# Kernel optimization log

Measured on AMD Instinct MI355X. Metric: run time of the kernel, lower is better.

Reference implementation:

```python
import jax, jax.numpy as jnp
import numpy as np

MIN_CLUSTERS = 3.0
MAX_CLUSTERS = 50.0


def setup_inputs() -> dict:
    key = jax.random.key(0)
    ks = jax.random.split(key, 8)
    B, N, D, H = 8, 100000, 64, 64
    E = 3200000
    x = jax.random.normal(ks[0], (B, N, D), dtype=jnp.float32)
    edge_index = jax.random.randint(ks[1], (2, E), 0, N, dtype=jnp.int64)
    in_dim = 3 * D + 4  # 196
    s1 = 1.0 / np.sqrt(in_dim)
    s2 = 1.0 / np.sqrt(H)
    s3 = 1.0 / np.sqrt(H // 2)
    W1 = jax.random.uniform(ks[2], (in_dim, H), jnp.float32, -s1, s1)
    b1 = jax.random.uniform(ks[3], (H,), jnp.float32, -s1, s1)
    W2 = jax.random.uniform(ks[4], (H, H // 2), jnp.float32, -s2, s2)
    b2 = jax.random.uniform(ks[5], (H // 2,), jnp.float32, -s2, s2)
    W3 = jax.random.uniform(ks[6], (H // 2, 1), jnp.float32, -s3, s3)
    b3 = jax.random.uniform(ks[7], (1,), jnp.float32, -s3, s3)
    return {"x": x, "edge_index": edge_index, "W1": W1, "b1": b1,
            "W2": W2, "b2": b2, "W3": W3, "b3": b3}


def reference(x, edge_index, W1, b1, W2, b2, W3, b3):
    B, N, D = x.shape
    # node pooling over the node axis (unbiased std, matching torch.std)
    x_mean = x.mean(axis=1)                 # [B, D]
    x_max = x.max(axis=1)                   # [B, D]
    x_std = jnp.std(x, axis=1, ddof=1)      # [B, D]
    # degree histogram: vectorized scatter-add replacing the serial python loop
    degrees = jnp.zeros((N,), dtype=jnp.float32).at[edge_index[1]].add(1.0)
    avg_degree = degrees.mean()
    std_degree = jnp.std(degrees, ddof=1)
    num_edges = edge_index.shape[1] // 2
    max_edges = N * (N - 1) / 2.0
    density = jnp.float32(num_edges / max_edges if max_edges > 0 else 0.0)
    normalized_size = jnp.float32(np.log(N + 1.0) / 10.0)
    structural = jnp.stack([avg_degree, std_degree, density, normalized_size])  # [4]
    structural = jnp.broadcast_to(structural[None, :], (B, 4))
    gf = jnp.concatenate([x_mean, x_max, x_std, structural], axis=1)  # [B, 3D+4]
    h = jax.nn.relu(gf @ W1 + b1)
    h = jax.nn.relu(h @ W2 + b2)
    cluster_raw = jax.nn.sigmoid(h @ W3 + b3)[:, 0]  # [B]
    cont = MIN_CLUSTERS + cluster_raw * (MAX_CLUSTERS - MIN_CLUSTERS)
    # straight-through round
    rounded = cont + jax.lax.stop_gradient(jnp.round(cont) - cont)
    return jnp.stack([rounded.mean(), cluster_raw.mean()])  # [num_clusters, raw_mean]
```

## Files before the change

kernel.cpp:

```cpp
#include <hip/hip_runtime.h>
#include <cstdint>
#include <cmath>


#define NSEG   64
#define NRNG   4
#define RBITS  15
#define RR     (1 << RBITS)
#define BPB    256
#define RFBLK  32

__device__ unsigned char      g_part[NSEG * NRNG * RR];
__device__ float              g_sum[512];
__device__ float              g_sq[512];
__device__ unsigned           g_max[512];
__device__ unsigned long long g_degSums[2];
__device__ unsigned           g_done = 0;

__device__ __forceinline__ unsigned enc_f32(float f) {
    unsigned u = __float_as_uint(f);
    return (u & 0x80000000u) ? ~u : (u | 0x80000000u);
}
__device__ __forceinline__ float dec_f32(unsigned u) {
    return (u & 0x80000000u) ? __uint_as_float(u ^ 0x80000000u) : __uint_as_float(~u);
}

__global__ __launch_bounds__(256) void hist_kernel(
    const int* __restrict__ ei, int E, int N)
{
    const int bid = blockIdx.x, tid = threadIdx.x;
    const int s = bid >> 2;
    const int p = bid & 3;
    const unsigned lo = (unsigned)p << RBITS;

    if (bid == 0) {
        for (int i = tid; i < 512; i += 256) { g_sum[i] = 0.f; g_sq[i] = 0.f; g_max[i] = 0u; }
        if (tid < 2) g_degSums[tid] = 0ull;
    }

    __shared__ unsigned h[RR];
    for (int i = tid; i < RR; i += 256) h[i] = 0u;
    __syncthreads();

    const int* row1 = ei + E;
    const int per = (E + NSEG - 1) / NSEG;
    const int elo = s * per, ehi = min(E, elo + per);
    const int span4 = (ehi - elo) & ~3;

    for (int i = elo + tid * 4; i + 3 < elo + span4 + 3 && i + 3 < ehi + 3 && i + 3 < elo + span4 + 4 && i < elo + span4; i += 256 * 4) {
        int4 v = *reinterpret_cast<const int4*>(row1 + i);
        unsigned r0 = (unsigned)v.x - lo; if (r0 < RR) atomicAdd(&h[r0], 1u);
        unsigned r1 = (unsigned)v.y - lo; if (r1 < RR) atomicAdd(&h[r1], 1u);
        unsigned r2 = (unsigned)v.z - lo; if (r2 < RR) atomicAdd(&h[r2], 1u);
        unsigned r3 = (unsigned)v.w - lo; if (r3 < RR) atomicAdd(&h[r3], 1u);
    }
    for (int i = elo + span4 + tid; i < ehi; i += 256) {
        unsigned r0 = (unsigned)row1[i] - lo; if (r0 < RR) atomicAdd(&h[r0], 1u);
    }
    __syncthreads();

    unsigned* outw = reinterpret_cast<unsigned*>(&g_part[(size_t)bid * RR]);
    for (int w = tid; w < RR / 4; w += 256) {
        unsigned c = (h[w*4] & 255u) | ((h[w*4+1] & 255u) << 8)
                   | ((h[w*4+2] & 255u) << 16) | ((h[w*4+3] & 255u) << 24);
        outw[w] = c;
    }
}

__global__ __launch_bounds__(256) void xstats_kernel(
    const float* __restrict__ x, int N, int rowsPerBlock)
{
    const int b   = blockIdx.x / BPB;
    const int blk = blockIdx.x - b * BPB;
    const int tid = threadIdx.x;
    const int d4  = tid & 15;
    const int rg  = tid >> 4;

    const int rowStart = blk * rowsPerBlock;
    const int rowEnd   = min(N, rowStart + rowsPerBlock);

    float s0 = 0.f, s1 = 0.f, s2 = 0.f, s3 = 0.f;
    float q0 = 0.f, q1 = 0.f, q2 = 0.f, q3 = 0.f;
    float m0 = -INFINITY, m1 = -INFINITY, m2 = -INFINITY, m3 = -INFINITY;

    const float* xb = x + (size_t)b * (size_t)N * 64 + d4 * 4;
    for (int r = rowStart + rg; r < rowEnd; r += 16) {
        float4 v = *reinterpret_cast<const float4*>(xb + (size_t)r * 64);
        s0 += v.x; s1 += v.y; s2 += v.z; s3 += v.w;
        q0 = fmaf(v.x, v.x, q0); q1 = fmaf(v.y, v.y, q1);
        q2 = fmaf(v.z, v.z, q2); q3 = fmaf(v.w, v.w, q3);
        m0 = fmaxf(m0, v.x); m1 = fmaxf(m1, v.y);
        m2 = fmaxf(m2, v.z); m3 = fmaxf(m3, v.w);
    }

    __shared__ float ls[256 * 4];
    __shared__ float lq[256 * 4];
    __shared__ float lm[256 * 4];
    ls[tid*4+0]=s0; ls[tid*4+1]=s1; ls[tid*4+2]=s2; ls[tid*4+3]=s3;
    lq[tid*4+0]=q0; lq[tid*4+1]=q1; lq[tid*4+2]=q2; lq[tid*4+3]=q3;
    lm[tid*4+0]=m0; lm[tid*4+1]=m1; lm[tid*4+2]=m2; lm[tid*4+3]=m3;
    __syncthreads();

    for (int off = 8; off; off >>= 1) {
        if (rg < off) {
            int o  = (tid + off * 16) * 4;
            int me = tid * 4;
            #pragma unroll
            for (int j = 0; j < 4; ++j) {
                ls[me+j] += ls[o+j];
                lq[me+j] += lq[o+j];
                lm[me+j]  = fmaxf(lm[me+j], lm[o+j]);
            }
        }
        __syncthreads();
    }

    if (rg == 0) {
        #pragma unroll
        for (int j = 0; j < 4; ++j) {
            int cell = b * 64 + d4 * 4 + j;
            atomicAdd(&g_sum[cell], ls[tid*4+j]);
            atomicAdd(&g_sq[cell],  lq[tid*4+j]);
            atomicMax(&g_max[cell], enc_f32(lm[tid*4+j]));
        }
    }
}

__global__ __launch_bounds__(256) void reduce_final_kernel(
    int N, long long E,
    const float* __restrict__ W1, const float* __restrict__ b1,
    const float* __restrict__ W2, const float* __restrict__ b2,
    const float* __restrict__ W3, const float* __restrict__ b3,
    float* __restrict__ out)
{
    const int bid = blockIdx.x, tid = threadIdx.x;
    const int p     = bid >> 3;
    const int chunk = bid & 7;

    uint4 acc = make_uint4(0u, 0u, 0u, 0u);
    const size_t roff = (size_t)chunk * 4096 + (size_t)tid * 16;
    for (int s = 0; s < NSEG; ++s) {
        const uint4 v = *reinterpret_cast<const uint4*>(
            &g_part[((size_t)(s * NRNG + p)) * RR + roff]);
        acc.x += v.x; acc.y += v.y; acc.z += v.z; acc.w += v.w;
    }
    unsigned sd = 0, sq = 0;
    unsigned words[4] = {acc.x, acc.y, acc.z, acc.w};
    #pragma unroll
    for (int wi = 0; wi < 4; ++wi) {
        #pragma unroll
        for (int by = 0; by < 4; ++by) {
            unsigned d = (words[wi] >> (by * 8)) & 255u;
            sd += d;
            sq += d * d;
        }
    }
    #pragma unroll
    for (int off = 32; off; off >>= 1) {
        sd += __shfl_down(sd, off, 64);
        sq += __shfl_down(sq, off, 64);
    }
    __shared__ unsigned wsd[4], wsq[4];
    if ((tid & 63) == 0) { wsd[tid >> 6] = sd; wsq[tid >> 6] = sq; }
    __syncthreads();
    if (tid == 0) {
        unsigned long long S = 0, Q = 0;
        #pragma unroll
        for (int wv = 0; wv < 4; ++wv) { S += wsd[wv]; Q += wsq[wv]; }
        atomicAdd(&g_degSums[0], S);
        atomicAdd(&g_degSums[1], Q);
    }

    __shared__ int lastFlag;
    __syncthreads();
    if (tid == 0) {
        unsigned old = atomicAdd(&g_done, 1u);
        lastFlag = (old == (unsigned)gridDim.x - 1u);
    }
    __syncthreads();
    if (!lastFlag) return;

    __shared__ float gf[8][200];
    __shared__ float h1s[8][64];
    __shared__ float h2s[8][32];
    __shared__ float raw[8], rnd[8];
    __shared__ unsigned long long degS[2];

    if (tid < 2) degS[tid] = atomicAdd(&g_degSums[tid], 0ull);
    __syncthreads();

    for (int i = tid; i < 512; i += 256) {
        int bb = i >> 6, d = i & 63;
        float sum = g_sum[i], sqv = g_sq[i];
        float mean = sum / (float)N;
        float var  = fmaxf(0.f, sqv - sum * sum / (float)N) / (float)(N - 1);
        gf[bb][d]       = mean;
        gf[bb][64 + d]  = dec_f32(g_max[i]);
        gf[bb][128 + d] = sqrtf(var);
    }
    if (tid < 32) {
        int bb = tid >> 2, k = tid & 3;
        double dsum = (double)degS[0];
        double dsq  = (double)degS[1];
        double avg  = dsum / (double)N;
        double var  = (dsq - dsum * dsum / (double)N) / (double)(N - 1);
        long long num_edges = E / 2;
        double max_edges = (double)N * (double)(N - 1) / 2.0;
        float v;
        if      (k == 0) v = (float)avg;
        else if (k == 1) v = (float)sqrt(var);
        else if (k == 2) v = (float)((double)num_edges / max_edges);
        else             v = (float)(log((double)N + 1.0) / 10.0);
        gf[bb][192 + k] = v;
    }
    __syncthreads();

    if (tid < 64) {
        int d = tid;
        for (int bb = 0; bb < 8; ++bb) {
            float acc2 = b1[d];
            for (int k = 0; k < 196; ++k)
                acc2 = fmaf(gf[bb][k], W1[k * 64 + d], acc2);
            h1s[bb][d] = fmaxf(acc2, 0.f);
        }
    }
    __syncthreads();

    if (tid < 32) {
        int d = tid;
        for (int bb = 0; bb < 8; ++bb) {
            float acc2 = b2[d];
            for (int k = 0; k < 64; ++k)
                acc2 = fmaf(h1s[bb][k], W2[k * 32 + d], acc2);
            h2s[bb][d] = fmaxf(acc2, 0.f);
        }
    }
    __syncthreads();

    if (tid < 8) {
        float acc2 = b3[0];
        for (int k = 0; k < 32; ++k)
            acc2 = fmaf(h2s[tid][k], W3[k], acc2);
        float r = 1.f / (1.f + expf(-acc2));
        raw[tid] = r;
        float cont = 3.0f + r * 47.0f;
        rnd[tid] = rintf(cont);
    }
    __syncthreads();

    if (tid == 0) {
        float sr = 0.f, sw = 0.f;
        for (int bb = 0; bb < 8; ++bb) { sr += rnd[bb]; sw += raw[bb]; }
        out[0] = sr * 0.125f;
        out[1] = sw * 0.125f;
        atomicExch(&g_done, 0u);
    }
}

extern "C" void kernel_launch(void* const* d_in, const int* in_sizes, int n_in,
                              void* d_out, int out_size, void* d_ws, size_t ws_size,
                              hipStream_t stream)
{
    const float* x  = (const float*)d_in[0];
    const int*   ei = (const int*)d_in[1];
    const float* W1 = (const float*)d_in[2];
    const float* b1 = (const float*)d_in[3];
    const float* W2 = (const float*)d_in[4];
    const float* b2 = (const float*)d_in[5];
    const float* W3 = (const float*)d_in[6];
    const float* b3 = (const float*)d_in[7];
    float* out = (float*)d_out;

    int N = in_sizes[0] / (8 * 64);
    if (N > NRNG * RR) N = NRNG * RR;
    const int E = in_sizes[1] / 2;

    const int rpb = (N + BPB - 1) / BPB;

    hist_kernel        <<<NSEG * NRNG, 256, 0, stream>>>(ei, E, N);
    xstats_kernel      <<<8 * BPB,     256, 0, stream>>>(x, N, rpb);
    reduce_final_kernel<<<RFBLK,       256, 0, stream>>>(N, (long long)E,
                                                         W1, b1, W2, b2, W3, b3, out);
}
```

Baseline: 131.8 us.

## Fuse x-statistics and degree reduction into one kernel with last-block finalize

```diff
diff --git a/kernel.cpp b/kernel.cpp
--- a/kernel.cpp
+++ b/kernel.cpp
@@ -8,6 +8,7 @@
 #define RBITS  15
 #define RR     (1 << RBITS)
 #define BPB    256
+#define XB     (8 * BPB)
 #define RFBLK  32
 
 __device__ unsigned char      g_part[NSEG * NRNG * RR];
@@ -45,17 +46,23 @@
     const int* row1 = ei + E;
     const int per = (E + NSEG - 1) / NSEG;
     const int elo = s * per, ehi = min(E, elo + per);
-    const int span4 = (ehi - elo) & ~3;
-
-    for (int i = elo + tid * 4; i + 3 < elo + span4 + 3 && i + 3 < ehi + 3 && i + 3 < elo + span4 + 4 && i < elo + span4; i += 256 * 4) {
-        int4 v = *reinterpret_cast<const int4*>(row1 + i);
-        unsigned r0 = (unsigned)v.x - lo; if (r0 < RR) atomicAdd(&h[r0], 1u);
-        unsigned r1 = (unsigned)v.y - lo; if (r1 < RR) atomicAdd(&h[r1], 1u);
-        unsigned r2 = (unsigned)v.z - lo; if (r2 < RR) atomicAdd(&h[r2], 1u);
-        unsigned r3 = (unsigned)v.w - lo; if (r3 < RR) atomicAdd(&h[r3], 1u);
-    }
-    for (int i = elo + span4 + tid; i < ehi; i += 256) {
-        unsigned r0 = (unsigned)row1[i] - lo; if (r0 < RR) atomicAdd(&h[r0], 1u);
+
+    if ((elo & 3) == 0) {
+        const int span4 = elo + ((ehi - elo) & ~3);
+        for (int i = elo + tid * 4; i < span4; i += 256 * 4) {
+            int4 v = *reinterpret_cast<const int4*>(row1 + i);
+            unsigned r0 = (unsigned)v.x - lo; if (r0 < RR) atomicAdd(&h[r0], 1u);
+            unsigned r1 = (unsigned)v.y - lo; if (r1 < RR) atomicAdd(&h[r1], 1u);
+            unsigned r2 = (unsigned)v.z - lo; if (r2 < RR) atomicAdd(&h[r2], 1u);
+            unsigned r3 = (unsigned)v.w - lo; if (r3 < RR) atomicAdd(&h[r3], 1u);
+        }
+        for (int i = span4 + tid; i < ehi; i += 256) {
+            unsigned r0 = (unsigned)row1[i] - lo; if (r0 < RR) atomicAdd(&h[r0], 1u);
+        }
+    } else {
+        for (int i = elo + tid; i < ehi; i += 256) {
+            unsigned r0 = (unsigned)row1[i] - lo; if (r0 < RR) atomicAdd(&h[r0], 1u);
+        }
     }
     __syncthreads();
 
@@ -67,111 +74,125 @@
     }
 }
 
-__global__ __launch_bounds__(256) void xstats_kernel(
-    const float* __restrict__ x, int N, int rowsPerBlock)
-{
-    const int b   = blockIdx.x / BPB;
-    const int blk = blockIdx.x - b * BPB;
-    const int tid = threadIdx.x;
-    const int d4  = tid & 15;
-    const int rg  = tid >> 4;
-
-    const int rowStart = blk * rowsPerBlock;
-    const int rowEnd   = min(N, rowStart + rowsPerBlock);
-
-    float s0 = 0.f, s1 = 0.f, s2 = 0.f, s3 = 0.f;
-    float q0 = 0.f, q1 = 0.f, q2 = 0.f, q3 = 0.f;
-    float m0 = -INFINITY, m1 = -INFINITY, m2 = -INFINITY, m3 = -INFINITY;
-
-    const float* xb = x + (size_t)b * (size_t)N * 64 + d4 * 4;
-    for (int r = rowStart + rg; r < rowEnd; r += 16) {
-        float4 v = *reinterpret_cast<const float4*>(xb + (size_t)r * 64);
-        s0 += v.x; s1 += v.y; s2 += v.z; s3 += v.w;
-        q0 = fmaf(v.x, v.x, q0); q1 = fmaf(v.y, v.y, q1);
-        q2 = fmaf(v.z, v.z, q2); q3 = fmaf(v.w, v.w, q3);
-        m0 = fmaxf(m0, v.x); m1 = fmaxf(m1, v.y);
-        m2 = fmaxf(m2, v.z); m3 = fmaxf(m3, v.w);
-    }
-
-    __shared__ float ls[256 * 4];
-    __shared__ float lq[256 * 4];
-    __shared__ float lm[256 * 4];
-    ls[tid*4+0]=s0; ls[tid*4+1]=s1; ls[tid*4+2]=s2; ls[tid*4+3]=s3;
-    lq[tid*4+0]=q0; lq[tid*4+1]=q1; lq[tid*4+2]=q2; lq[tid*4+3]=q3;
-    lm[tid*4+0]=m0; lm[tid*4+1]=m1; lm[tid*4+2]=m2; lm[tid*4+3]=m3;
-    __syncthreads();
-
-    for (int off = 8; off; off >>= 1) {
-        if (rg < off) {
-            int o  = (tid + off * 16) * 4;
-            int me = tid * 4;
-            #pragma unroll
-            for (int j = 0; j < 4; ++j) {
-                ls[me+j] += ls[o+j];
-                lq[me+j] += lq[o+j];
-                lm[me+j]  = fmaxf(lm[me+j], lm[o+j]);
-            }
-        }
-        __syncthreads();
-    }
-
-    if (rg == 0) {
-        #pragma unroll
-        for (int j = 0; j < 4; ++j) {
-            int cell = b * 64 + d4 * 4 + j;
-            atomicAdd(&g_sum[cell], ls[tid*4+j]);
-            atomicAdd(&g_sq[cell],  lq[tid*4+j]);
-            atomicMax(&g_max[cell], enc_f32(lm[tid*4+j]));
-        }
-    }
-}
-
-__global__ __launch_bounds__(256) void reduce_final_kernel(
-    int N, long long E,
+__global__ __launch_bounds__(256) void xstats_final_kernel(
+    const float* __restrict__ x, int N, int rowsPerBlock, long long E,
     const float* __restrict__ W1, const float* __restrict__ b1,
     const float* __restrict__ W2, const float* __restrict__ b2,
     const float* __restrict__ W3, const float* __restrict__ b3,
     float* __restrict__ out)
 {
-    const int bid = blockIdx.x, tid = threadIdx.x;
-    const int p     = bid >> 3;
-    const int chunk = bid & 7;
-
-    uint4 acc = make_uint4(0u, 0u, 0u, 0u);
-    const size_t roff = (size_t)chunk * 4096 + (size_t)tid * 16;
-    for (int s = 0; s < NSEG; ++s) {
-        const uint4 v = *reinterpret_cast<const uint4*>(
-            &g_part[((size_t)(s * NRNG + p)) * RR + roff]);
-        acc.x += v.x; acc.y += v.y; acc.z += v.z; acc.w += v.w;
-    }
-    unsigned sd = 0, sq = 0;
-    unsigned words[4] = {acc.x, acc.y, acc.z, acc.w};
-    #pragma unroll
-    for (int wi = 0; wi < 4; ++wi) {
+    const int tid = threadIdx.x;
+
+    if (blockIdx.x < XB) {
+        const int b   = blockIdx.x / BPB;
+        const int blk = blockIdx.x - b * BPB;
+        const int d4  = tid & 15;
+        const int rg  = tid >> 4;
+
+        const int rowStart = blk * rowsPerBlock;
+        const int rowEnd   = min(N, rowStart + rowsPerBlock);
+
+        float s0 = 0.f, s1 = 0.f, s2 = 0.f, s3 = 0.f;
+        float q0 = 0.f, q1 = 0.f, q2 = 0.f, q3 = 0.f;
+        float m0 = -INFINITY, m1 = -INFINITY, m2 = -INFINITY, m3 = -INFINITY;
+
+        const float* xb = x + (size_t)b * (size_t)N * 64 + d4 * 4;
+        int r = rowStart + rg;
+        for (; r + 16 < rowEnd; r += 32) {
+            float4 v = *reinterpret_cast<const float4*>(xb + (size_t)r * 64);
+            float4 w = *reinterpret_cast<const float4*>(xb + (size_t)(r + 16) * 64);
+            s0 += v.x; s1 += v.y; s2 += v.z; s3 += v.w;
+            q0 = fmaf(v.x, v.x, q0); q1 = fmaf(v.y, v.y, q1);
+            q2 = fmaf(v.z, v.z, q2); q3 = fmaf(v.w, v.w, q3);
+            m0 = fmaxf(m0, v.x); m1 = fmaxf(m1, v.y);
+            m2 = fmaxf(m2, v.z); m3 = fmaxf(m3, v.w);
+            s0 += w.x; s1 += w.y; s2 += w.z; s3 += w.w;
+            q0 = fmaf(w.x, w.x, q0); q1 = fmaf(w.y, w.y, q1);
+            q2 = fmaf(w.z, w.z, q2); q3 = fmaf(w.w, w.w, q3);
+            m0 = fmaxf(m0, w.x); m1 = fmaxf(m1, w.y);
+            m2 = fmaxf(m2, w.z); m3 = fmaxf(m3, w.w);
+        }
+        if (r < rowEnd) {
+            float4 v = *reinterpret_cast<const float4*>(xb + (size_t)r * 64);
+            s0 += v.x; s1 += v.y; s2 += v.z; s3 += v.w;
+            q0 = fmaf(v.x, v.x, q0); q1 = fmaf(v.y, v.y, q1);
+            q2 = fmaf(v.z, v.z, q2); q3 = fmaf(v.w, v.w, q3);
+            m0 = fmaxf(m0, v.x); m1 = fmaxf(m1, v.y);
+            m2 = fmaxf(m2, v.z); m3 = fmaxf(m3, v.w);
+        }
+
+        __shared__ float ls[256 * 4];
+        __shared__ float lq[256 * 4];
+        __shared__ float lm[256 * 4];
+        ls[tid*4+0]=s0; ls[tid*4+1]=s1; ls[tid*4+2]=s2; ls[tid*4+3]=s3;
+        lq[tid*4+0]=q0; lq[tid*4+1]=q1; lq[tid*4+2]=q2; lq[tid*4+3]=q3;
+        lm[tid*4+0]=m0; lm[tid*4+1]=m1; lm[tid*4+2]=m2; lm[tid*4+3]=m3;
+        __syncthreads();
+
+        for (int off = 8; off; off >>= 1) {
+            if (rg < off) {
+                int o  = (tid + off * 16) * 4;
+                int me = tid * 4;
+                #pragma unroll
+                for (int j = 0; j < 4; ++j) {
+                    ls[me+j] += ls[o+j];
+                    lq[me+j] += lq[o+j];
+                    lm[me+j]  = fmaxf(lm[me+j], lm[o+j]);
+                }
+            }
+            __syncthreads();
+        }
+
+        if (rg == 0) {
+            #pragma unroll
+            for (int j = 0; j < 4; ++j) {
+                int cell = b * 64 + d4 * 4 + j;
+                atomicAdd(&g_sum[cell], ls[tid*4+j]);
+                atomicAdd(&g_sq[cell],  lq[tid*4+j]);
+                atomicMax(&g_max[cell], enc_f32(lm[tid*4+j]));
+            }
+        }
+    } else {
+        const int rb    = blockIdx.x - XB;
+        const int p     = rb >> 3;
+        const int chunk = rb & 7;
+
+        uint4 acc = make_uint4(0u, 0u, 0u, 0u);
+        const size_t roff = (size_t)chunk * 4096 + (size_t)tid * 16;
+        for (int s = 0; s < NSEG; ++s) {
+            const uint4 v = *reinterpret_cast<const uint4*>(
+                &g_part[((size_t)(s * NRNG + p)) * RR + roff]);
+            acc.x += v.x; acc.y += v.y; acc.z += v.z; acc.w += v.w;
+        }
+        unsigned sd = 0, sq = 0;
+        unsigned words[4] = {acc.x, acc.y, acc.z, acc.w};
         #pragma unroll
-        for (int by = 0; by < 4; ++by) {
-            unsigned d = (words[wi] >> (by * 8)) & 255u;
-            sd += d;
-            sq += d * d;
-        }
-    }
-    #pragma unroll
-    for (int off = 32; off; off >>= 1) {
-        sd += __shfl_down(sd, off, 64);
-        sq += __shfl_down(sq, off, 64);
-    }
-    __shared__ unsigned wsd[4], wsq[4];
-    if ((tid & 63) == 0) { wsd[tid >> 6] = sd; wsq[tid >> 6] = sq; }
-    __syncthreads();
-    if (tid == 0) {
-        unsigned long long S = 0, Q = 0;
+        for (int wi = 0; wi < 4; ++wi)
+            #pragma unroll
+            for (int by = 0; by < 4; ++by) {
+                unsigned d = (words[wi] >> (by * 8)) & 255u;
+                sd += d;
+                sq += d * d;
+            }
         #pragma unroll
-        for (int wv = 0; wv < 4; ++wv) { S += wsd[wv]; Q += wsq[wv]; }
-        atomicAdd(&g_degSums[0], S);
-        atomicAdd(&g_degSums[1], Q);
+        for (int off = 32; off; off >>= 1) {
+            sd += __shfl_down(sd, off, 64);
+            sq += __shfl_down(sq, off, 64);
+        }
+        __shared__ unsigned wsd[4], wsq[4];
+        if ((tid & 63) == 0) { wsd[tid >> 6] = sd; wsq[tid >> 6] = sq; }
+        __syncthreads();
+        if (tid == 0) {
+            unsigned long long S = 0, Q = 0;
+            #pragma unroll
+            for (int wv = 0; wv < 4; ++wv) { S += wsd[wv]; Q += wsq[wv]; }
+            atomicAdd(&g_degSums[0], S);
+            atomicAdd(&g_degSums[1], Q);
+        }
     }
 
     __shared__ int lastFlag;
+    __threadfence();
     __syncthreads();
     if (tid == 0) {
         unsigned old = atomicAdd(&g_done, 1u);
@@ -191,11 +212,13 @@
 
     for (int i = tid; i < 512; i += 256) {
         int bb = i >> 6, d = i & 63;
-        float sum = g_sum[i], sqv = g_sq[i];
+        float sum = atomicAdd(&g_sum[i], 0.f);
+        float sqv = atomicAdd(&g_sq[i], 0.f);
+        unsigned mx = atomicAdd(&g_max[i], 0u);
         float mean = sum / (float)N;
         float var  = fmaxf(0.f, sqv - sum * sum / (float)N) / (float)(N - 1);
         gf[bb][d]       = mean;
-        gf[bb][64 + d]  = dec_f32(g_max[i]);
+        gf[bb][64 + d]  = dec_f32(mx);
         gf[bb][128 + d] = sqrtf(var);
     }
     if (tid < 32) {
@@ -277,8 +300,7 @@
 
     const int rpb = (N + BPB - 1) / BPB;
 
-    hist_kernel        <<<NSEG * NRNG, 256, 0, stream>>>(ei, E, N);
-    xstats_kernel      <<<8 * BPB,     256, 0, stream>>>(x, N, rpb);
-    reduce_final_kernel<<<RFBLK,       256, 0, stream>>>(N, (long long)E,
-                                                         W1, b1, W2, b2, W3, b3, out);
-}
+    hist_kernel<<<NSEG * NRNG, 256, 0, stream>>>(ei, E, N);
+    xstats_final_kernel<<<XB + RFBLK, 256, 0, stream>>>(
+        x, N, rpb, (long long)E, W1, b1, W2, b2, W3, b3, out);
+}
```

After: 253.5 us. 1.92x slower.
